# Kernel tuning notes

Hardware: AMD Instinct MI355X
Metric: run time of the kernel (lower is better)

## Reference

```python
import jax, jax.numpy as jnp
import numpy as np

D_MODEL = 1024
H = 16
DK = 64  # d_model // h
M = 8    # memory slots
NQ = 1024
B = 8


def setup_inputs() -> dict:
    key = jax.random.key(0)
    ks = jax.random.split(key, 10)
    f = lambda k, s, sc=1.0: jax.random.normal(k, s, dtype=jnp.float32) * sc
    return {
        "queries": f(ks[0], (NQ, B, D_MODEL)),
        "keys": f(ks[1], (NQ, B, D_MODEL)),
        "values": f(ks[2], (NQ, B, D_MODEL)),
        "m_k": f(ks[3], (1, M, D_MODEL), 0.1),
        "m_v": f(ks[4], (1, M, D_MODEL), 0.1),
        "attn_mask": f(ks[5], (B, H, NQ, NQ), 0.02),  # additive float mask over real keys
        "in_proj_weight": f(ks[6], (3 * D_MODEL, D_MODEL), 0.02),
        "in_proj_bias": jnp.zeros((3 * D_MODEL,), jnp.float32),
        "out_w": f(ks[7], (D_MODEL, D_MODEL), 0.02),
        "out_b": jnp.zeros((D_MODEL,), jnp.float32),
    }


def _fp16(w):
    # The torch module casts projection weights/biases to fp16 before linear.
    return w.astype(jnp.float16).astype(jnp.float32)


def reference(queries, keys, values, m_k, m_v, attn_mask,
              in_proj_weight, in_proj_bias, out_w, out_b):
    # (seq, batch, d) -> (batch, seq, d)
    q_in = queries.transpose(1, 0, 2)
    k_in = keys.transpose(1, 0, 2)
    v_in = values.transpose(1, 0, 2)
    b, nq, d = q_in.shape
    nk = k_in.shape[1]
    m = m_k.shape[1]

    w_q, w_k, w_v = jnp.split(in_proj_weight, 3, axis=0)
    b_q, b_k, b_v = jnp.split(in_proj_bias, 3)

    q = q_in @ _fp16(w_q).T + _fp16(b_q)
    k = k_in @ _fp16(w_k).T + _fp16(b_k)
    v = v_in @ _fp16(w_v).T + _fp16(b_v)

    # scaled learnable memory slots, broadcast over batch
    mk = float(np.sqrt(DK * H)) * jnp.broadcast_to(m_k, (b, m, d))
    mv = float(np.sqrt(m)) * jnp.broadcast_to(m_v, (b, m, d))
    k = jnp.concatenate([k, mk], axis=1)  # (b, nk+m, d)
    v = jnp.concatenate([v, mv], axis=1)

    qh = q.reshape(b, nq, H, DK).transpose(0, 2, 1, 3)        # (b,h,nq,dk)
    kh = k.reshape(b, nk + m, H, DK).transpose(0, 2, 3, 1)    # (b,h,dk,nk+m)
    vh = v.reshape(b, nk + m, H, DK).transpose(0, 2, 1, 3)    # (b,h,nk+m,dv)

    att = jnp.matmul(qh, kh) / float(np.sqrt(DK))             # (b,h,nq,nk+m)
    # additive mask applies only to the real keys, memory slots unmasked
    mask_pad = jnp.concatenate(
        [attn_mask, jnp.zeros((b, H, nq, m), att.dtype)], axis=-1)
    att = jax.nn.softmax(att + mask_pad, axis=-1)

    out = jnp.matmul(att, vh).transpose(0, 2, 1, 3).reshape(b, nq, H * DK)
    out = out @ out_w.T + out_b
    return out.transpose(1, 0, 2)  # back to (seq, batch, d)
```

## Files before the change

kernel.cpp:

```cpp
#include <hip/hip_runtime.h>
#include <cstdint>

typedef _Float16 half8  __attribute__((ext_vector_type(8)));
typedef _Float16 half4v __attribute__((ext_vector_type(4)));
typedef float    f32x4  __attribute__((ext_vector_type(4)));

#define MFMA_F16(a,b,c) __builtin_amdgcn_mfma_f32_16x16x32_f16(a,b,c,0,0,0)

static constexpr int D = 1024, H = 16, DK = 64, BATCH = 8, NQ = 1024;
static constexpr int NKP = 1040;

__device__ __forceinline__ void async_copy16(_Float16* lds, const _Float16* g) {
  __builtin_amdgcn_global_load_lds(
      (const __attribute__((address_space(1))) void*)g,
      (__attribute__((address_space(3))) void*)lds, 16, 0, 0);
}

__global__ __launch_bounds__(256) void convert_all(
    const float* __restrict__ q, const float* __restrict__ k, const float* __restrict__ v,
    const float* __restrict__ w_in, const float* __restrict__ w_out,
    _Float16* __restrict__ q16, _Float16* __restrict__ k16, _Float16* __restrict__ v16,
    _Float16* __restrict__ win16, _Float16* __restrict__ wout16)
{
  const unsigned NA = 8192u * 1024u;
  const unsigned NW = 3u * 1024u * 1024u;
  unsigned idx = blockIdx.x * 256u + threadIdx.x;
  unsigned e = idx * 8u;
  const float* src;
  _Float16* dst;
  unsigned off;
  if (e < NA)            { src = q;     dst = q16;    off = e; }
  else if (e < 2 * NA)   { src = k;     dst = k16;    off = e - NA; }
  else if (e < 3 * NA)   { src = v;     dst = v16;    off = e - 2 * NA; }
  else if (e < 3 * NA + NW) { src = w_in; dst = win16; off = e - 3 * NA; }
  else                   { src = w_out; dst = wout16; off = e - 3 * NA - NW; }
  float4 f0 = ((const float4*)(src + off))[0];
  float4 f1 = ((const float4*)(src + off))[1];
  half8 h;
  h[0]=(_Float16)f0.x; h[1]=(_Float16)f0.y; h[2]=(_Float16)f0.z; h[3]=(_Float16)f0.w;
  h[4]=(_Float16)f1.x; h[5]=(_Float16)f1.y; h[6]=(_Float16)f1.z; h[7]=(_Float16)f1.w;
  *(half8*)(dst + off) = h;
}

__global__ __launch_bounds__(256) void gemm_qkv(
    const _Float16* __restrict__ A16,
    const _Float16* __restrict__ W16,
    const float* __restrict__ bias,
    _Float16* __restrict__ Qo, _Float16* __restrict__ Ko, _Float16* __restrict__ Vo)
{
  const int z = blockIdx.z;
  const _Float16* __restrict__ A = A16 + (size_t)z * 8192 * 1024;
  const _Float16* __restrict__ Wz = W16 + (size_t)z * D * D;
  const int row0 = blockIdx.x * 128;
  const int col0 = blockIdx.y * 128;

  __shared__ _Float16 As[128 * 32];
  __shared__ _Float16 Bs[128 * 32];

  const int tid = threadIdx.x;
  const int wv = tid >> 6, lane = tid & 63, c = lane & 15, g = lane >> 4;
  const int ar0 = (wv & 1) * 64, bc0 = (wv >> 1) * 64;

  const int srow = 32 * wv + (lane >> 2);
  const int sk8 = (lane & 3) * 8;
  const _Float16* ag = A + (size_t)(row0 + srow) * D + sk8;
  const _Float16* bg = Wz + (size_t)(col0 + srow) * D + sk8;
  _Float16* al = &As[(32 * wv) * 32];
  _Float16* bl = &Bs[(32 * wv) * 32];

  f32x4 acc[4][4];
#pragma unroll
  for (int i = 0; i < 4; i++)
#pragma unroll
    for (int j = 0; j < 4; j++) acc[i][j] = (f32x4)(0.f);

  for (int kb = 0; kb < D; kb += 32) {
    async_copy16(al,           ag + kb);
    async_copy16(al + 16 * 32, ag + kb + (size_t)16 * D);
    async_copy16(bl,           bg + kb);
    async_copy16(bl + 16 * 32, bg + kb + (size_t)16 * D);
    __syncthreads();
    half8 af[4], bf[4];
#pragma unroll
    for (int i = 0; i < 4; i++) af[i] = *(const half8*)&As[(ar0 + 16 * i + c) * 32 + 8 * g];
#pragma unroll
    for (int j = 0; j < 4; j++) bf[j] = *(const half8*)&Bs[(bc0 + 16 * j + c) * 32 + 8 * g];
#pragma unroll
    for (int i = 0; i < 4; i++)
#pragma unroll
      for (int j = 0; j < 4; j++) acc[i][j] = MFMA_F16(af[i], bf[j], acc[i][j]);
    __syncthreads();
  }

#pragma unroll
  for (int j = 0; j < 4; j++) {
    int n = col0 + bc0 + 16 * j + c;
    float bb = (float)(_Float16)bias[z * D + n];
    int h_ = n >> 6, dk = n & 63;
#pragma unroll
    for (int i = 0; i < 4; i++) {
#pragma unroll
      for (int r = 0; r < 4; r++) {
        int m = row0 + ar0 + 16 * i + 4 * g + r;
        int b = m & 7, nq = m >> 3;
        float val = acc[i][j][r] + bb;
        if (z == 0)
          Qo[(((size_t)b * H + h_) * NQ + nq) * DK + dk] = (_Float16)(val * 0.125f);
        else if (z == 1)
          Ko[(((size_t)b * H + h_) * NKP + nq) * DK + dk] = (_Float16)val;
        else
          Vo[(((size_t)b * H + h_) * NKP + nq) * DK + dk] = (_Float16)val;
      }
    }
  }
}

__global__ __launch_bounds__(256) void fill_slots(
    const float* __restrict__ mk, const float* __restrict__ mv,
    _Float16* __restrict__ Ko, _Float16* __restrict__ Vo)
{
  int idx = blockIdx.x * 256 + threadIdx.x;
  int which = idx >> 17;
  int e = idx & 131071;
  int dk = e & 63, r = (e >> 6) & 15, h = (e >> 10) & 15, b = (e >> 14) & 7;
  float val = 0.f;
  if (r < 8) {
    int src = r * D + h * DK + dk;
    val = which ? 2.8284271247461903f * mv[src] : 32.f * mk[src];
  }
  _Float16* dst = which ? Vo : Ko;
  dst[(((size_t)b * H + h) * NKP + 1024 + r) * DK + dk] = (_Float16)val;
}

__global__ __launch_bounds__(256) void attn(
    const _Float16* __restrict__ Qg, const _Float16* __restrict__ Kg,
    const _Float16* __restrict__ Vg, const float* __restrict__ mask,
    _Float16* __restrict__ Hid)
{
  const int qt = blockIdx.x;
  const int bh = blockIdx.y;
  const int b = bh >> 4, h = bh & 15;
  const int tid = threadIdx.x;
  const int wv = tid >> 6, lane = tid & 63, c = lane & 15, g = lane >> 4;

  __shared__ _Float16 Qs[64 * 72];
  __shared__ _Float16 Ks[64 * 72];
  __shared__ _Float16 Vt[64 * 72];
  __shared__ _Float16 Ps[64 * 72];

  const _Float16* qbase = Qg + ((size_t)bh * NQ + qt * 64) * DK;
#pragma unroll
  for (int u = 0; u < 2; u++) {
    int id = tid + 256 * u;
    int row = id >> 3, m8 = (id & 7) * 8;
    *(int4*)&Qs[row * 72 + m8] = *(const int4*)(qbase + row * DK + m8);
  }
  __syncthreads();
  const int qrow = (wv * 16 + c) * 72;
  half8 qf0 = *(const half8*)&Qs[qrow + 8 * g];
  half8 qf1 = *(const half8*)&Qs[qrow + 32 + 8 * g];

  f32x4 oacc[4];
#pragma unroll
  for (int j = 0; j < 4; j++) oacc[j] = (f32x4)(0.f);
  float lpart = 0.f;

  const float* maskbase = mask + ((size_t)bh << 20) + ((size_t)(qt * 64 + wv * 16 + c) << 10);
  const _Float16* kbase_g = Kg + (size_t)bh * NKP * DK;
  const _Float16* vbase_g = Vg + (size_t)bh * NKP * DK;

  for (int ci = 0; ci < 17; ++ci) {
    const int kb = ci * 64;
    const int nk = (ci < 16) ? 64 : 16;
    __syncthreads();

    f32x4 sinit[4];
    if (ci < 16) {
#pragma unroll
      for (int t = 0; t < 4; t++)
        sinit[t] = *(const f32x4*)(maskbase + kb + 16 * t + 4 * g);
    } else {
      float iv = (g < 2) ? 0.f : -1e30f;
      sinit[0] = (f32x4){iv, iv, iv, iv};
    }

#pragma unroll
    for (int u = 0; u < 2; u++) {
      int id = tid + 256 * u;
      int row = id >> 3, m8 = (id & 7) * 8;
      if (row < nk)
        *(int4*)&Ks[row * 72 + m8] = *(const int4*)(kbase_g + (size_t)(kb + row) * DK + m8);
    }
    {
      int kp = tid & 31, dvo = (tid >> 5) * 8;
      if (2 * kp < nk) {
        uint4 a4 = *(const uint4*)(vbase_g + (size_t)(kb + 2 * kp) * DK + dvo);
        uint4 b4 = *(const uint4*)(vbase_g + (size_t)(kb + 2 * kp + 1) * DK + dvo);
        uint32_t aw[4] = {a4.x, a4.y, a4.z, a4.w};
        uint32_t bw[4] = {b4.x, b4.y, b4.z, b4.w};
#pragma unroll
        for (int w = 0; w < 4; w++) {
          uint32_t lo = (aw[w] & 0xffffu) | (bw[w] << 16);
          uint32_t hi = (aw[w] >> 16) | (bw[w] & 0xffff0000u);
          *(uint32_t*)&Vt[(dvo + 2 * w) * 72 + 2 * kp] = lo;
          *(uint32_t*)&Vt[(dvo + 2 * w + 1) * 72 + 2 * kp] = hi;
        }
      } else if (nk == 16) {
#pragma unroll
        for (int w = 0; w < 4; w++) {
          *(uint32_t*)&Vt[(dvo + 2 * w) * 72 + 2 * kp] = 0u;
          *(uint32_t*)&Vt[(dvo + 2 * w + 1) * 72 + 2 * kp] = 0u;
        }
      }
    }
    __syncthreads();

    const int ntile = nk >> 4;
    for (int t = 0; t < ntile; ++t) {
      f32x4 s = sinit[t];
      half8 kf0 = *(const half8*)&Ks[(16 * t + c) * 72 + 8 * g];
      half8 kf1 = *(const half8*)&Ks[(16 * t + c) * 72 + 32 + 8 * g];
      s = MFMA_F16(kf0, qf0, s);
      s = MFMA_F16(kf1, qf1, s);
      f32x4 p;
      p[0] = __expf(s[0]); p[1] = __expf(s[1]); p[2] = __expf(s[2]); p[3] = __expf(s[3]);
      lpart += p[0] + p[1] + p[2] + p[3];
      half4v ph;
      ph[0] = (_Float16)p[0]; ph[1] = (_Float16)p[1];
      ph[2] = (_Float16)p[2]; ph[3] = (_Float16)p[3];
      *(half4v*)&Ps[qrow + 16 * t + 4 * g] = ph;
    }
    if (nk == 16) {
      half4v zz = {(_Float16)0, (_Float16)0, (_Float16)0, (_Float16)0};
      *(half4v*)&Ps[qrow + 16 + 4 * g] = zz;
    }

    const int khalf = (nk == 64) ? 2 : 1;
    for (int kh = 0; kh < khalf; ++kh) {
      half8 pf = *(const half8*)&Ps[qrow + 32 * kh + 8 * g];
#pragma unroll
      for (int j = 0; j < 4; j++) {
        half8 vf = *(const half8*)&Vt[(16 * j + c) * 72 + 32 * kh + 8 * g];
        oacc[j] = MFMA_F16(pf, vf, oacc[j]);
      }
    }
  }

  lpart += __shfl_xor(lpart, 16);
  lpart += __shfl_xor(lpart, 32);
  float inv_[4];
#pragma unroll
  for (int r = 0; r < 4; r++) {
    float lq = __shfl(lpart, 4 * g + r);
    inv_[r] = __builtin_amdgcn_rcpf(lq);
  }
#pragma unroll
  for (int j = 0; j < 4; j++) {
    int col = h * DK + 16 * j + c;
#pragma unroll
    for (int r = 0; r < 4; r++) {
      int q = qt * 64 + wv * 16 + 4 * g + r;
      Hid[((size_t)q * BATCH + b) * D + col] = (_Float16)(oacc[j][r] * inv_[r]);
    }
  }
}

__global__ __launch_bounds__(256) void gemm_out(
    const _Float16* __restrict__ Ah, const _Float16* __restrict__ W16,
    const float* __restrict__ bias, float* __restrict__ Out)
{
  const int row0 = blockIdx.x * 128, col0 = blockIdx.y * 128;
  __shared__ _Float16 As[128 * 32];
  __shared__ _Float16 Bs[128 * 32];
  const int tid = threadIdx.x;
  const int wv = tid >> 6, lane = tid & 63, c = lane & 15, g = lane >> 4;
  const int ar0 = (wv & 1) * 64, bc0 = (wv >> 1) * 64;

  const int srow = 32 * wv + (lane >> 2);
  const int sk8 = (lane & 3) * 8;
  const _Float16* ag = Ah + (size_t)(row0 + srow) * D + sk8;
  const _Float16* bg = W16 + (size_t)(col0 + srow) * D + sk8;
  _Float16* al = &As[(32 * wv) * 32];
  _Float16* bl = &Bs[(32 * wv) * 32];

  f32x4 acc[4][4];
#pragma unroll
  for (int i = 0; i < 4; i++)
#pragma unroll
    for (int j = 0; j < 4; j++) acc[i][j] = (f32x4)(0.f);

  for (int kb = 0; kb < D; kb += 32) {
    async_copy16(al,           ag + kb);
    async_copy16(al + 16 * 32, ag + kb + (size_t)16 * D);
    async_copy16(bl,           bg + kb);
    async_copy16(bl + 16 * 32, bg + kb + (size_t)16 * D);
    __syncthreads();
    half8 af[4], bf[4];
#pragma unroll
    for (int i = 0; i < 4; i++) af[i] = *(const half8*)&As[(ar0 + 16 * i + c) * 32 + 8 * g];
#pragma unroll
    for (int j = 0; j < 4; j++) bf[j] = *(const half8*)&Bs[(bc0 + 16 * j + c) * 32 + 8 * g];
#pragma unroll
    for (int i = 0; i < 4; i++)
#pragma unroll
      for (int j = 0; j < 4; j++) acc[i][j] = MFMA_F16(af[i], bf[j], acc[i][j]);
    __syncthreads();
  }

#pragma unroll
  for (int j = 0; j < 4; j++) {
    int n = col0 + bc0 + 16 * j + c;
    float bb = bias[n];
#pragma unroll
    for (int i = 0; i < 4; i++) {
#pragma unroll
      for (int r = 0; r < 4; r++) {
        int m = row0 + ar0 + 16 * i + 4 * g + r;
        Out[(size_t)m * D + n] = acc[i][j][r] + bb;
      }
    }
  }
}

extern "C" void kernel_launch(void* const* d_in, const int* in_sizes, int n_in,
                              void* d_out, int out_size, void* d_ws, size_t ws_size,
                              hipStream_t stream) {
  const float* queries   = (const float*)d_in[0];
  const float* keys      = (const float*)d_in[1];
  const float* values    = (const float*)d_in[2];
  const float* m_k       = (const float*)d_in[3];
  const float* m_v       = (const float*)d_in[4];
  const float* attn_mask = (const float*)d_in[5];
  const float* in_proj_w = (const float*)d_in[6];
  const float* in_proj_b = (const float*)d_in[7];
  const float* out_w     = (const float*)d_in[8];
  const float* out_b     = (const float*)d_in[9];
  float* out = (float*)d_out;

  const size_t NA = (size_t)8192 * 1024;
  _Float16* A16  = (_Float16*)d_ws;
  _Float16* Win16  = A16 + 3 * NA;
  _Float16* Wout16 = Win16 + (size_t)3 * 1024 * 1024;
  _Float16* Qw = Wout16 + (size_t)1024 * 1024;
  _Float16* Kw = Qw + (size_t)8 * 16 * 1024 * 64;
  _Float16* Vw = Kw + (size_t)8 * 16 * 1040 * 64;
  _Float16* Hw = Vw + (size_t)8 * 16 * 1040 * 64;

  hipLaunchKernelGGL(convert_all, dim3(14336), dim3(256), 0, stream,
                     queries, keys, values, in_proj_w, out_w,
                     A16, A16 + NA, A16 + 2 * NA, Win16, Wout16);
  hipLaunchKernelGGL(gemm_qkv, dim3(64, 8, 3), dim3(256), 0, stream,
                     A16, Win16, in_proj_b, Qw, Kw, Vw);
  hipLaunchKernelGGL(fill_slots, dim3(1024), dim3(256), 0, stream, m_k, m_v, Kw, Vw);
  hipLaunchKernelGGL(attn, dim3(16, 128), dim3(256), 0, stream, Qw, Kw, Vw, attn_mask, Hw);
  hipLaunchKernelGGL(gemm_out, dim3(64, 8), dim3(256), 0, stream, Hw, Wout16, out_b, out);
}
```

Measured before the change: 948.2 us.

## Deepen GEMM K-tile with swizzled LDS and double attention query tile per block

Both GEMMs now stage a 64-wide K slice per iteration instead of 32. They use an XOR swizzle on the LDS column offset to avoid bank conflicts, which halves barrier count per K. The attention kernel processes 128 queries per block with 512 threads, so each K/V chunk loaded into LDS is reused by twice as many query rows. Q and P share one LDS buffer. Larger blocks reduce occupancy flexibility and change how the load work is split across threads.

Result: no change. 932.4 us (-1.7%).

```diff
diff --git a/kernel.cpp b/kernel.cpp
--- a/kernel.cpp
+++ b/kernel.cpp
@@ -54,19 +54,20 @@
   const int row0 = blockIdx.x * 128;
   const int col0 = blockIdx.y * 128;
 
-  __shared__ _Float16 As[128 * 32];
-  __shared__ _Float16 Bs[128 * 32];
+  __shared__ _Float16 As[128 * 64];
+  __shared__ _Float16 Bs[128 * 64];
 
   const int tid = threadIdx.x;
   const int wv = tid >> 6, lane = tid & 63, c = lane & 15, g = lane >> 4;
   const int ar0 = (wv & 1) * 64, bc0 = (wv >> 1) * 64;
-
-  const int srow = 32 * wv + (lane >> 2);
-  const int sk8 = (lane & 3) * 8;
+  const int cswz = (c & 7) << 3;
+
+  const int srow = tid >> 3;
+  const int sk8 = (((tid & 7) ^ ((tid >> 3) & 7)) << 3);
   const _Float16* ag = A + (size_t)(row0 + srow) * D + sk8;
   const _Float16* bg = Wz + (size_t)(col0 + srow) * D + sk8;
-  _Float16* al = &As[(32 * wv) * 32];
-  _Float16* bl = &Bs[(32 * wv) * 32];
+  _Float16* al = &As[512 * wv];
+  _Float16* bl = &Bs[512 * wv];
 
   f32x4 acc[4][4];
 #pragma unroll
@@ -74,21 +75,27 @@
 #pragma unroll
     for (int j = 0; j < 4; j++) acc[i][j] = (f32x4)(0.f);
 
-  for (int kb = 0; kb < D; kb += 32) {
-    async_copy16(al,           ag + kb);
-    async_copy16(al + 16 * 32, ag + kb + (size_t)16 * D);
-    async_copy16(bl,           bg + kb);
-    async_copy16(bl + 16 * 32, bg + kb + (size_t)16 * D);
-    __syncthreads();
-    half8 af[4], bf[4];
-#pragma unroll
-    for (int i = 0; i < 4; i++) af[i] = *(const half8*)&As[(ar0 + 16 * i + c) * 32 + 8 * g];
-#pragma unroll
-    for (int j = 0; j < 4; j++) bf[j] = *(const half8*)&Bs[(bc0 + 16 * j + c) * 32 + 8 * g];
-#pragma unroll
-    for (int i = 0; i < 4; i++)
-#pragma unroll
-      for (int j = 0; j < 4; j++) acc[i][j] = MFMA_F16(af[i], bf[j], acc[i][j]);
+  for (int kb = 0; kb < D; kb += 64) {
+#pragma unroll
+    for (int u = 0; u < 4; u++) {
+      async_copy16(al + 2048 * u, ag + kb + (size_t)(32 * u) * D);
+      async_copy16(bl + 2048 * u, bg + kb + (size_t)(32 * u) * D);
+    }
+    __syncthreads();
+#pragma unroll
+    for (int kk = 0; kk < 2; kk++) {
+      half8 af[4], bf[4];
+#pragma unroll
+      for (int i = 0; i < 4; i++)
+        af[i] = *(const half8*)&As[(ar0 + 16 * i + c) * 64 + ((32 * kk + 8 * g) ^ cswz)];
+#pragma unroll
+      for (int j = 0; j < 4; j++)
+        bf[j] = *(const half8*)&Bs[(bc0 + 16 * j + c) * 64 + ((32 * kk + 8 * g) ^ cswz)];
+#pragma unroll
+      for (int i = 0; i < 4; i++)
+#pragma unroll
+        for (int j = 0; j < 4; j++) acc[i][j] = MFMA_F16(af[i], bf[j], acc[i][j]);
+    }
     __syncthreads();
   }
 
@@ -132,7 +139,7 @@
   dst[(((size_t)b * H + h) * NKP + 1024 + r) * DK + dk] = (_Float16)val;
 }
 
-__global__ __launch_bounds__(256) void attn(
+__global__ __launch_bounds__(512) void attn(
     const _Float16* __restrict__ Qg, const _Float16* __restrict__ Kg,
     const _Float16* __restrict__ Vg, const float* __restrict__ mask,
     _Float16* __restrict__ Hid)
@@ -143,29 +150,28 @@
   const int tid = threadIdx.x;
   const int wv = tid >> 6, lane = tid & 63, c = lane & 15, g = lane >> 4;
 
-  __shared__ _Float16 Qs[64 * 72];
+  __shared__ _Float16 QPs[128 * 72];
   __shared__ _Float16 Ks[64 * 72];
   __shared__ _Float16 Vt[64 * 72];
-  __shared__ _Float16 Ps[64 * 72];
-
-  const _Float16* qbase = Qg + ((size_t)bh * NQ + qt * 64) * DK;
+
+  const _Float16* qbase = Qg + ((size_t)bh * NQ + qt * 128) * DK;
 #pragma unroll
   for (int u = 0; u < 2; u++) {
-    int id = tid + 256 * u;
+    int id = tid + 512 * u;
     int row = id >> 3, m8 = (id & 7) * 8;
-    *(int4*)&Qs[row * 72 + m8] = *(const int4*)(qbase + row * DK + m8);
+    *(int4*)&QPs[row * 72 + m8] = *(const int4*)(qbase + row * DK + m8);
   }
   __syncthreads();
   const int qrow = (wv * 16 + c) * 72;
-  half8 qf0 = *(const half8*)&Qs[qrow + 8 * g];
-  half8 qf1 = *(const half8*)&Qs[qrow + 32 + 8 * g];
+  half8 qf0 = *(const half8*)&QPs[qrow + 8 * g];
+  half8 qf1 = *(const half8*)&QPs[qrow + 32 + 8 * g];
 
   f32x4 oacc[4];
 #pragma unroll
   for (int j = 0; j < 4; j++) oacc[j] = (f32x4)(0.f);
   float lpart = 0.f;
 
-  const float* maskbase = mask + ((size_t)bh << 20) + ((size_t)(qt * 64 + wv * 16 + c) << 10);
+  const float* maskbase = mask + ((size_t)bh << 20) + ((size_t)(qt * 128 + wv * 16 + c) << 10);
   const _Float16* kbase_g = Kg + (size_t)bh * NKP * DK;
   const _Float16* vbase_g = Vg + (size_t)bh * NKP * DK;
 
@@ -184,14 +190,12 @@
       sinit[0] = (f32x4){iv, iv, iv, iv};
     }
 
-#pragma unroll
-    for (int u = 0; u < 2; u++) {
-      int id = tid + 256 * u;
-      int row = id >> 3, m8 = (id & 7) * 8;
+    {
+      int row = tid >> 3, m8 = (tid & 7) * 8;
       if (row < nk)
         *(int4*)&Ks[row * 72 + m8] = *(const int4*)(kbase_g + (size_t)(kb + row) * DK + m8);
     }
-    {
+    if (tid < 256) {
       int kp = tid & 31, dvo = (tid >> 5) * 8;
       if (2 * kp < nk) {
         uint4 a4 = *(const uint4*)(vbase_g + (size_t)(kb + 2 * kp) * DK + dvo);
@@ -228,16 +232,16 @@
       half4v ph;
       ph[0] = (_Float16)p[0]; ph[1] = (_Float16)p[1];
       ph[2] = (_Float16)p[2]; ph[3] = (_Float16)p[3];
-      *(half4v*)&Ps[qrow + 16 * t + 4 * g] = ph;
+      *(half4v*)&QPs[qrow + 16 * t + 4 * g] = ph;
     }
     if (nk == 16) {
       half4v zz = {(_Float16)0, (_Float16)0, (_Float16)0, (_Float16)0};
-      *(half4v*)&Ps[qrow + 16 + 4 * g] = zz;
+      *(half4v*)&QPs[qrow + 16 + 4 * g] = zz;
     }
 
     const int khalf = (nk == 64) ? 2 : 1;
     for (int kh = 0; kh < khalf; ++kh) {
-      half8 pf = *(const half8*)&Ps[qrow + 32 * kh + 8 * g];
+      half8 pf = *(const half8*)&QPs[qrow + 32 * kh + 8 * g];
 #pragma unroll
       for (int j = 0; j < 4; j++) {
         half8 vf = *(const half8*)&Vt[(16 * j + c) * 72 + 32 * kh + 8 * g];
@@ -259,7 +263,7 @@
     int col = h * DK + 16 * j + c;
 #pragma unroll
     for (int r = 0; r < 4; r++) {
-      int q = qt * 64 + wv * 16 + 4 * g + r;
+      int q = qt * 128 + wv * 16 + 4 * g + r;
       Hid[((size_t)q * BATCH + b) * D + col] = (_Float16)(oacc[j][r] * inv_[r]);
     }
   }
@@ -270,18 +274,19 @@
     const float* __restrict__ bias, float* __restrict__ Out)
 {
   const int row0 = blockIdx.x * 128, col0 = blockIdx.y * 128;
-  __shared__ _Float16 As[128 * 32];
-  __shared__ _Float16 Bs[128 * 32];
+  __shared__ _Float16 As[128 * 64];
+  __shared__ _Float16 Bs[128 * 64];
   const int tid = threadIdx.x;
   const int wv = tid >> 6, lane = tid & 63, c = lane & 15, g = lane >> 4;
   const int ar0 = (wv & 1) * 64, bc0 = (wv >> 1) * 64;
-
-  const int srow = 32 * wv + (lane >> 2);
-  const int sk8 = (lane & 3) * 8;
+  const int cswz = (c & 7) << 3;
+
+  const int srow = tid >> 3;
+  const int sk8 = (((tid & 7) ^ ((tid >> 3) & 7)) << 3);
   const _Float16* ag = Ah + (size_t)(row0 + srow) * D + sk8;
   const _Float16* bg = W16 + (size_t)(col0 + srow) * D + sk8;
-  _Float16* al = &As[(32 * wv) * 32];
-  _Float16* bl = &Bs[(32 * wv) * 32];
+  _Float16* al = &As[512 * wv];
+  _Float16* bl = &Bs[512 * wv];
 
   f32x4 acc[4][4];
 #pragma unroll
@@ -289,21 +294,27 @@
 #pragma unroll
     for (int j = 0; j < 4; j++) acc[i][j] = (f32x4)(0.f);
 
-  for (int kb = 0; kb < D; kb += 32) {
-    async_copy16(al,           ag + kb);
-    async_copy16(al + 16 * 32, ag + kb + (size_t)16 * D);
-    async_copy16(bl,           bg + kb);
-    async_copy16(bl + 16 * 32, bg + kb + (size_t)16 * D);
-    __syncthreads();
-    half8 af[4], bf[4];
-#pragma unroll
-    for (int i = 0; i < 4; i++) af[i] = *(const half8*)&As[(ar0 + 16 * i + c) * 32 + 8 * g];
-#pragma unroll
-    for (int j = 0; j < 4; j++) bf[j] = *(const half8*)&Bs[(bc0 + 16 * j + c) * 32 + 8 * g];
-#pragma unroll
-    for (int i = 0; i < 4; i++)
-#pragma unroll
-      for (int j = 0; j < 4; j++) acc[i][j] = MFMA_F16(af[i], bf[j], acc[i][j]);
+  for (int kb = 0; kb < D; kb += 64) {
+#pragma unroll
+    for (int u = 0; u < 4; u++) {
+      async_copy16(al + 2048 * u, ag + kb + (size_t)(32 * u) * D);
+      async_copy16(bl + 2048 * u, bg + kb + (size_t)(32 * u) * D);
+    }
+    __syncthreads();
+#pragma unroll
+    for (int kk = 0; kk < 2; kk++) {
+      half8 af[4], bf[4];
+#pragma unroll
+      for (int i = 0; i < 4; i++)
+        af[i] = *(const half8*)&As[(ar0 + 16 * i + c) * 64 + ((32 * kk + 8 * g) ^ cswz)];
+#pragma unroll
+      for (int j = 0; j < 4; j++)
+        bf[j] = *(const half8*)&Bs[(bc0 + 16 * j + c) * 64 + ((32 * kk + 8 * g) ^ cswz)];
+#pragma unroll
+      for (int i = 0; i < 4; i++)
+#pragma unroll
+        for (int j = 0; j < 4; j++) acc[i][j] = MFMA_F16(af[i], bf[j], acc[i][j]);
+    }
     __syncthreads();
   }
 
@@ -352,6 +363,6 @@
   hipLaunchKernelGGL(gemm_qkv, dim3(64, 8, 3), dim3(256), 0, stream,
                      A16, Win16, in_proj_b, Qw, Kw, Vw);
   hipLaunchKernelGGL(fill_slots, dim3(1024), dim3(256), 0, stream, m_k, m_v, Kw, Vw);
-  hipLaunchKernelGGL(attn, dim3(16, 128), dim3(256), 0, stream, Qw, Kw, Vw, attn_mask, Hw);
+  hipLaunchKernelGGL(attn, dim3(8, 128), dim3(512), 0, stream, Qw, Kw, Vw, attn_mask, Hw);
   hipLaunchKernelGGL(gemm_out, dim3(64, 8), dim3(256), 0, stream, Hw, Wout16, out_b, out);
 }
```
